# Kernel tuning notes

Hardware: AMD Instinct MI355X
Metric: run time of the kernel (lower is better)

## Reference

```python
import jax, jax.numpy as jnp
import numpy as np

B, T, F, H = 4096, 128, 64, 32
SCALE = 0.05  # small init so relu-LSTM doesn't blow up over 128 steps


def setup_inputs() -> dict:
    key = jax.random.key(0)
    ks = jax.random.split(key, 7)
    return {
        "x": jax.random.normal(ks[0], (B, T, F), jnp.float32),
        "We": jax.random.normal(ks[1], (F, 4 * H), jnp.float32) * SCALE,
        "Ue": jax.random.normal(ks[2], (H, 4 * H), jnp.float32) * SCALE,
        "be": jnp.zeros((4 * H,), jnp.float32),
        "Wd": jax.random.normal(ks[3], (H, 4 * H), jnp.float32) * SCALE,
        "Ud": jax.random.normal(ks[4], (H, 4 * H), jnp.float32) * SCALE,
        "bd": jnp.zeros((4 * H,), jnp.float32),
        "Wout": jax.random.normal(ks[5], (H, F), jnp.float32) * SCALE,
        "bout": jnp.zeros((F,), jnp.float32),
    }


def _lstm_relu(x, W, U, b):
    """Keras LSTM with activation='relu', recurrent_activation='sigmoid'.
    x: [B,T,D]. Returns (h_T [B,H], h_seq [B,T,H]). Gate order: i,f,c,o."""
    Bx = x.shape[0]
    Hh = U.shape[0]
    xz = jnp.einsum('btd,dg->btg', x, W) + b  # precompute input projections

    def step(carry, zt):
        h, c = carry
        z = zt + h @ U
        i, f, g, o = jnp.split(z, 4, axis=-1)
        i = jax.nn.sigmoid(i)
        f = jax.nn.sigmoid(f)
        g = jax.nn.relu(g)
        o = jax.nn.sigmoid(o)
        c = f * c + i * g
        h = o * jax.nn.relu(c)
        return (h, c), h

    h0 = jnp.zeros((Bx, Hh), x.dtype)
    (hT, _), hs = jax.lax.scan(step, (h0, h0), jnp.swapaxes(xz, 0, 1))
    return hT, jnp.swapaxes(hs, 0, 1)


def reference(x, We, Ue, be, Wd, Ud, bd, Wout, bout):
    # Encoder: LSTM(32, relu, return_sequences=False) -> RepeatVector(T)
    hT, _ = _lstm_relu(x, We, Ue, be)                      # [B,H]
    z = jnp.broadcast_to(hT[:, None, :], (x.shape[0], x.shape[1], hT.shape[-1]))
    # Decoder: LSTM(32, relu, return_sequences=True) -> TimeDistributed(Dense(F))
    _, hs = _lstm_relu(z, Wd, Ud, bd)                      # [B,T,H]
    return jnp.einsum('bth,hf->btf', hs, Wout) + bout      # [B,T,F]
```

## Files before the change

### kernel.cpp

```cpp
#include <hip/hip_runtime.h>
#include <hip/hip_bf16.h>

#define B_ 4096
#define T_ 128
#define F_ 64
#define H_ 32
#define G_ 128

using short8 = __attribute__((ext_vector_type(8))) short;
using f32x4  = __attribute__((ext_vector_type(4))) float;
using uint2v = __attribute__((ext_vector_type(2))) unsigned int;
using uint4v = __attribute__((ext_vector_type(4))) unsigned int;

#define MFMA16(Af, Bf, Cf) __builtin_amdgcn_mfma_f32_16x16x32_bf16((Af), (Bf), (Cf), 0, 0, 0)

__device__ __forceinline__ float sigmoid_f(float z) {
    return __builtin_amdgcn_rcpf(1.0f + __expf(-z));
}
__device__ __forceinline__ unsigned short bfb(float f) {
    return __builtin_bit_cast(unsigned short, __float2bfloat16(f));
}
__device__ __forceinline__ unsigned int pk(float a, float b) {
    return (unsigned int)bfb(a) | ((unsigned int)bfb(b) << 16);
}

extern "C" __global__ __launch_bounds__(128, 1)
void lstm_ae(const float* __restrict__ x,
             const float* __restrict__ We,
             const float* __restrict__ Ue,
             const float* __restrict__ be,
             const float* __restrict__ Wd,
             const float* __restrict__ Ud,
             const float* __restrict__ bd,
             const float* __restrict__ Wout,
             const float* __restrict__ bout,
             float* __restrict__ out)
{
    const int lane = threadIdx.x & 63;
    const int rw   = threadIdx.x >> 6;
    const int g    = lane >> 4;
    const int c    = lane & 15;
    const int b0   = blockIdx.x << 4;

    __shared__ __align__(16) unsigned int hx[2][16 * 18];

    short8 weF[4][2];
    short8 ueF[4];
    f32x4  beC[4];
#pragma unroll
    for (int q = 0; q < 4; ++q) {
        const int n = 2 * q + rw;
#pragma unroll
        for (int kc = 0; kc < 2; ++kc)
#pragma unroll
            for (int i = 0; i < 8; ++i)
                weF[q][kc][i] = (short)bfb(We[(kc * 32 + 8 * g + i) * G_ + 16 * n + c]);
#pragma unroll
        for (int i = 0; i < 8; ++i)
            ueF[q][i] = (short)bfb(Ue[(4 * g + (i & 3) + 16 * (i >> 2)) * G_ + 16 * n + c]);
        beC[q] = *(const f32x4*)(be + 16 * n + 4 * g);
    }

    const float* xr = x + (size_t)(b0 + c) * (T_ * F_);
    const int xo = 8 * g;

    short8 hfrag = (short8)0;
    float  cs[4] = {0.f, 0.f, 0.f, 0.f};

#define CVTX(xf0, xf1)                                   \
    {                                                    \
        _Pragma("unroll")                                \
        for (int i = 0; i < 4; ++i) {                    \
            xf0[i]     = (short)bfb(xa[i]);              \
            xf0[4 + i] = (short)bfb(xb[i]);              \
            xf1[i]     = (short)bfb(xc[i]);              \
            xf1[4 + i] = (short)bfb(xd[i]);              \
        }                                                \
    }

#define GATES4(ACC, OWN)                                 \
    {                                                    \
        float hv[4];                                     \
        _Pragma("unroll")                                \
        for (int r = 0; r < 4; ++r) {                    \
            float iv = sigmoid_f(ACC[0][r]);             \
            float fv = sigmoid_f(ACC[1][r]);             \
            float gv = fmaxf(ACC[2][r], 0.f);            \
            float ov = sigmoid_f(ACC[3][r]);             \
            float cc = fmaf(fv, cs[r], iv * gv);         \
            cs[r] = cc;                                  \
            hv[r] = ov * fmaxf(cc, 0.f);                 \
        }                                                \
        OWN.x = pk(hv[0], hv[1]);                        \
        OWN.y = pk(hv[2], hv[3]);                        \
    }

    f32x4 xa = *(const f32x4*)(xr + xo);
    f32x4 xb = *(const f32x4*)(xr + xo + 4);
    f32x4 xc = *(const f32x4*)(xr + 32 + xo);
    f32x4 xd = *(const f32x4*)(xr + 36 + xo);
    short8 xf0, xf1;
    CVTX(xf0, xf1)
    {
        const float* xn = xr + F_;
        xa = *(const f32x4*)(xn + xo);
        xb = *(const f32x4*)(xn + xo + 4);
        xc = *(const f32x4*)(xn + 32 + xo);
        xd = *(const f32x4*)(xn + 36 + xo);
    }
    f32x4 acc[4];
#pragma unroll
    for (int q = 0; q < 4; ++q) {
        acc[q] = MFMA16(weF[q][0], xf0, beC[q]);
        acc[q] = MFMA16(weF[q][1], xf1, acc[q]);
    }

#pragma unroll 1
    for (int t = 0; t < T_; ++t) {
#pragma unroll
        for (int q = 0; q < 4; ++q)
            acc[q] = MFMA16(ueF[q], hfrag, acc[q]);
        uint2v own;
        GATES4(acc, own)
        *(uint2v*)&hx[t & 1][c * 18 + 8 * rw + 2 * g] = own;
        __syncthreads();

        uint2v oth = *(const uint2v*)&hx[t & 1][c * 18 + 8 * (1 - rw) + 2 * g];
        if (t + 1 < T_) {
            CVTX(xf0, xf1)
            if (t + 2 < T_) {
                const float* xn = xr + (t + 2) * F_;
                xa = *(const f32x4*)(xn + xo);
                xb = *(const f32x4*)(xn + xo + 4);
                xc = *(const f32x4*)(xn + 32 + xo);
                xd = *(const f32x4*)(xn + 36 + xo);
            }
#pragma unroll
            for (int q = 0; q < 4; ++q) {
                acc[q] = MFMA16(weF[q][0], xf0, beC[q]);
                acc[q] = MFMA16(weF[q][1], xf1, acc[q]);
            }
        }
        uint4v hb;
        hb.x = rw ? oth.x : own.x;
        hb.y = rw ? oth.y : own.y;
        hb.z = rw ? own.x : oth.x;
        hb.w = rw ? own.y : oth.y;
        hfrag = __builtin_bit_cast(short8, hb);
    }

    short8 udF[4], woF[2];
    f32x4  zd[4], boC[2];
    {
        short8 wdF[4];
#pragma unroll
        for (int q = 0; q < 4; ++q) {
            const int n = 2 * q + rw;
#pragma unroll
            for (int i = 0; i < 8; ++i) {
                const int pr = 4 * g + (i & 3) + 16 * (i >> 2);
                wdF[q][i] = (short)bfb(Wd[pr * G_ + 16 * n + c]);
                udF[q][i] = (short)bfb(Ud[pr * G_ + 16 * n + c]);
            }
        }
#pragma unroll
        for (int q = 0; q < 4; ++q) {
            f32x4 tb = *(const f32x4*)(bd + 16 * (2 * q + rw) + 4 * g);
            zd[q] = MFMA16(wdF[q], hfrag, tb);
        }
#pragma unroll
        for (int mi = 0; mi < 2; ++mi) {
            const int m = 2 * rw + mi;
#pragma unroll
            for (int i = 0; i < 8; ++i)
                woF[mi][i] = (short)bfb(Wout[(4 * g + (i & 3) + 16 * (i >> 2)) * F_ + 16 * m + c]);
            float v = bout[16 * m + c];
            boC[mi][0] = v; boC[mi][1] = v; boC[mi][2] = v; boC[mi][3] = v;
        }
    }

    hfrag = (short8)0;
#pragma unroll
    for (int r = 0; r < 4; ++r) cs[r] = 0.f;

    float* ob[4];
#pragma unroll
    for (int r = 0; r < 4; ++r)
        ob[r] = out + (size_t)(b0 + 4 * g + r) * (T_ * F_) + c;

#pragma unroll 1
    for (int t = 0; t < T_; ++t) {
#pragma unroll
        for (int q = 0; q < 4; ++q)
            acc[q] = MFMA16(udF[q], hfrag, zd[q]);
        uint2v own;
        GATES4(acc, own)
        *(uint2v*)&hx[t & 1][c * 18 + 8 * rw + 2 * g] = own;
        __syncthreads();

        uint2v oth = *(const uint2v*)&hx[t & 1][c * 18 + 8 * (1 - rw) + 2 * g];
        if (t > 0) {
#pragma unroll
            for (int mi = 0; mi < 2; ++mi) {
                f32x4 oac = MFMA16(hfrag, woF[mi], boC[mi]);
                const int m = 2 * rw + mi;
#pragma unroll
                for (int r = 0; r < 4; ++r)
                    ob[r][(t - 1) * F_ + 16 * m] = oac[r];
            }
        }
        uint4v hb;
        hb.x = rw ? oth.x : own.x;
        hb.y = rw ? oth.y : own.y;
        hb.z = rw ? own.x : oth.x;
        hb.w = rw ? own.y : oth.y;
        hfrag = __builtin_bit_cast(short8, hb);
    }
#pragma unroll
    for (int mi = 0; mi < 2; ++mi) {
        f32x4 oac = MFMA16(hfrag, woF[mi], boC[mi]);
        const int m = 2 * rw + mi;
#pragma unroll
        for (int r = 0; r < 4; ++r)
            ob[r][(T_ - 1) * F_ + 16 * m] = oac[r];
    }
}

extern "C" void kernel_launch(void* const* d_in, const int* in_sizes, int n_in,
                              void* d_out, int out_size, void* d_ws, size_t ws_size,
                              hipStream_t stream) {
    (void)in_sizes; (void)n_in; (void)d_ws; (void)ws_size; (void)out_size;
    const float* x    = (const float*)d_in[0];
    const float* We   = (const float*)d_in[1];
    const float* Ue   = (const float*)d_in[2];
    const float* be   = (const float*)d_in[3];
    const float* Wd   = (const float*)d_in[4];
    const float* Ud   = (const float*)d_in[5];
    const float* bd   = (const float*)d_in[6];
    const float* Wout = (const float*)d_in[7];
    const float* bout = (const float*)d_in[8];
    float* out = (float*)d_out;

    dim3 grid(B_ / 16), block(128);
    hipLaunchKernelGGL(lstm_ae, grid, block, 0, stream,
                       x, We, Ue, be, Wd, Ud, bd, Wout, bout, out);
}
```

Before: 392.8 us.

## Split gate nonlinearities across four waves per block with lighter barrier

Raises the block from two to four waves. Each pair of waves computes the same gate MFMAs redundantly, and each wave then evaluates the nonlinearities for only two of the four accumulator rows. This halves the per-wave serial gate and transcendental work on the recurrent critical path. The shared h exchange becomes a single 16-byte read of all four waves' words. The __syncthreads is replaced by an explicit lgkmcnt wait plus s_barrier, and the output projection is split so each wave does one 16-column MFMA. The cost is duplicated MFMA and x-load work, and more registers and waves per block.

```diff
diff --git a/kernel.cpp b/kernel.cpp
--- a/kernel.cpp
+++ b/kernel.cpp
@@ -9,7 +9,6 @@
 
 using short8 = __attribute__((ext_vector_type(8))) short;
 using f32x4  = __attribute__((ext_vector_type(4))) float;
-using uint2v = __attribute__((ext_vector_type(2))) unsigned int;
 using uint4v = __attribute__((ext_vector_type(4))) unsigned int;
 
 #define MFMA16(Af, Bf, Cf) __builtin_amdgcn_mfma_f32_16x16x32_bf16((Af), (Bf), (Cf), 0, 0, 0)
@@ -24,7 +23,14 @@
     return (unsigned int)bfb(a) | ((unsigned int)bfb(b) << 16);
 }
 
-extern "C" __global__ __launch_bounds__(128, 1)
+#define XBAR()                                                  \
+    {                                                           \
+        asm volatile("s_waitcnt lgkmcnt(0)" ::: "memory");      \
+        __builtin_amdgcn_s_barrier();                           \
+        __builtin_amdgcn_sched_barrier(0);                      \
+    }
+
+extern "C" __global__ __launch_bounds__(256, 1)
 void lstm_ae(const float* __restrict__ x,
              const float* __restrict__ We,
              const float* __restrict__ Ue,
@@ -37,19 +43,21 @@
              float* __restrict__ out)
 {
     const int lane = threadIdx.x & 63;
-    const int rw   = threadIdx.x >> 6;
+    const int w    = threadIdx.x >> 6;
+    const int hw   = w >> 1;
+    const int rsel = w & 1;
     const int g    = lane >> 4;
     const int c    = lane & 15;
     const int b0   = blockIdx.x << 4;
 
-    __shared__ __align__(16) unsigned int hx[2][16 * 18];
+    __shared__ __align__(16) unsigned int hx[2][16 * 20];
 
     short8 weF[4][2];
     short8 ueF[4];
     f32x4  beC[4];
 #pragma unroll
     for (int q = 0; q < 4; ++q) {
-        const int n = 2 * q + rw;
+        const int n = 2 * q + hw;
 #pragma unroll
         for (int kc = 0; kc < 2; ++kc)
 #pragma unroll
@@ -65,7 +73,7 @@
     const int xo = 8 * g;
 
     short8 hfrag = (short8)0;
-    float  cs[4] = {0.f, 0.f, 0.f, 0.f};
+    float cs0 = 0.f, cs1 = 0.f;
 
 #define CVTX(xf0, xf1)                                   \
     {                                                    \
@@ -78,22 +86,25 @@
         }                                                \
     }
 
-#define GATES4(ACC, OWN)                                 \
+#define GATES2(R0, R1)                                   \
     {                                                    \
-        float hv[4];                                     \
-        _Pragma("unroll")                                \
-        for (int r = 0; r < 4; ++r) {                    \
-            float iv = sigmoid_f(ACC[0][r]);             \
-            float fv = sigmoid_f(ACC[1][r]);             \
-            float gv = fmaxf(ACC[2][r], 0.f);            \
-            float ov = sigmoid_f(ACC[3][r]);             \
-            float cc = fmaf(fv, cs[r], iv * gv);         \
-            cs[r] = cc;                                  \
-            hv[r] = ov * fmaxf(cc, 0.f);                 \
-        }                                                \
-        OWN.x = pk(hv[0], hv[1]);                        \
-        OWN.y = pk(hv[2], hv[3]);                        \
-    }
+        float iv0 = sigmoid_f(acc[0][R0]);               \
+        float fv0 = sigmoid_f(acc[1][R0]);               \
+        float gv0 = fmaxf(acc[2][R0], 0.f);              \
+        float ov0 = sigmoid_f(acc[3][R0]);               \
+        float cc0 = fmaf(fv0, cs0, iv0 * gv0);           \
+        cs0 = cc0;                                       \
+        float h0 = ov0 * fmaxf(cc0, 0.f);                \
+        float iv1 = sigmoid_f(acc[0][R1]);               \
+        float fv1 = sigmoid_f(acc[1][R1]);               \
+        float gv1 = fmaxf(acc[2][R1], 0.f);              \
+        float ov1 = sigmoid_f(acc[3][R1]);               \
+        float cc1 = fmaf(fv1, cs1, iv1 * gv1);           \
+        cs1 = cc1;                                       \
+        float h1 = ov1 * fmaxf(cc1, 0.f);                \
+        hword = pk(h0, h1);                              \
+    }
+#define GATES()  { if (rsel == 0) GATES2(0, 1) else GATES2(2, 3) }
 
     f32x4 xa = *(const f32x4*)(xr + xo);
     f32x4 xb = *(const f32x4*)(xr + xo + 4);
@@ -120,12 +131,11 @@
 #pragma unroll
         for (int q = 0; q < 4; ++q)
             acc[q] = MFMA16(ueF[q], hfrag, acc[q]);
-        uint2v own;
-        GATES4(acc, own)
-        *(uint2v*)&hx[t & 1][c * 18 + 8 * rw + 2 * g] = own;
-        __syncthreads();
-
-        uint2v oth = *(const uint2v*)&hx[t & 1][c * 18 + 8 * (1 - rw) + 2 * g];
+        unsigned int hword;
+        GATES()
+        hx[t & 1][c * 20 + 4 * g + w] = hword;
+        XBAR()
+        uint4v hb = *(const uint4v*)&hx[t & 1][c * 20 + 4 * g];
         if (t + 1 < T_) {
             CVTX(xf0, xf1)
             if (t + 2 < T_) {
@@ -141,21 +151,16 @@
                 acc[q] = MFMA16(weF[q][1], xf1, acc[q]);
             }
         }
-        uint4v hb;
-        hb.x = rw ? oth.x : own.x;
-        hb.y = rw ? oth.y : own.y;
-        hb.z = rw ? own.x : oth.x;
-        hb.w = rw ? own.y : oth.y;
         hfrag = __builtin_bit_cast(short8, hb);
     }
 
-    short8 udF[4], woF[2];
-    f32x4  zd[4], boC[2];
+    short8 udF[4], woF;
+    f32x4  zd[4], boC;
     {
         short8 wdF[4];
 #pragma unroll
         for (int q = 0; q < 4; ++q) {
-            const int n = 2 * q + rw;
+            const int n = 2 * q + hw;
 #pragma unroll
             for (int i = 0; i < 8; ++i) {
                 const int pr = 4 * g + (i & 3) + 16 * (i >> 2);
@@ -165,64 +170,47 @@
         }
 #pragma unroll
         for (int q = 0; q < 4; ++q) {
-            f32x4 tb = *(const f32x4*)(bd + 16 * (2 * q + rw) + 4 * g);
+            f32x4 tb = *(const f32x4*)(bd + 16 * (2 * q + hw) + 4 * g);
             zd[q] = MFMA16(wdF[q], hfrag, tb);
         }
 #pragma unroll
-        for (int mi = 0; mi < 2; ++mi) {
-            const int m = 2 * rw + mi;
-#pragma unroll
-            for (int i = 0; i < 8; ++i)
-                woF[mi][i] = (short)bfb(Wout[(4 * g + (i & 3) + 16 * (i >> 2)) * F_ + 16 * m + c]);
-            float v = bout[16 * m + c];
-            boC[mi][0] = v; boC[mi][1] = v; boC[mi][2] = v; boC[mi][3] = v;
-        }
+        for (int i = 0; i < 8; ++i)
+            woF[i] = (short)bfb(Wout[(4 * g + (i & 3) + 16 * (i >> 2)) * F_ + 16 * w + c]);
+        float v = bout[16 * w + c];
+        boC[0] = v; boC[1] = v; boC[2] = v; boC[3] = v;
     }
 
     hfrag = (short8)0;
-#pragma unroll
-    for (int r = 0; r < 4; ++r) cs[r] = 0.f;
+    cs0 = 0.f; cs1 = 0.f;
 
     float* ob[4];
 #pragma unroll
     for (int r = 0; r < 4; ++r)
-        ob[r] = out + (size_t)(b0 + 4 * g + r) * (T_ * F_) + c;
+        ob[r] = out + (size_t)(b0 + 4 * g + r) * (T_ * F_) + 16 * w + c;
 
 #pragma unroll 1
     for (int t = 0; t < T_; ++t) {
 #pragma unroll
         for (int q = 0; q < 4; ++q)
             acc[q] = MFMA16(udF[q], hfrag, zd[q]);
-        uint2v own;
-        GATES4(acc, own)
-        *(uint2v*)&hx[t & 1][c * 18 + 8 * rw + 2 * g] = own;
-        __syncthreads();
-
-        uint2v oth = *(const uint2v*)&hx[t & 1][c * 18 + 8 * (1 - rw) + 2 * g];
+        unsigned int hword;
+        GATES()
+        hx[t & 1][c * 20 + 4 * g + w] = hword;
+        XBAR()
+        uint4v hb = *(const uint4v*)&hx[t & 1][c * 20 + 4 * g];
         if (t > 0) {
-#pragma unroll
-            for (int mi = 0; mi < 2; ++mi) {
-                f32x4 oac = MFMA16(hfrag, woF[mi], boC[mi]);
-                const int m = 2 * rw + mi;
-#pragma unroll
-                for (int r = 0; r < 4; ++r)
-                    ob[r][(t - 1) * F_ + 16 * m] = oac[r];
-            }
-        }
-        uint4v hb;
-        hb.x = rw ? oth.x : own.x;
-        hb.y = rw ? oth.y : own.y;
-        hb.z = rw ? own.x : oth.x;
-        hb.w = rw ? own.y : oth.y;
+            f32x4 oac = MFMA16(hfrag, woF, boC);
+#pragma unroll
+            for (int r = 0; r < 4; ++r)
+                ob[r][(t - 1) * F_] = oac[r];
+        }
         hfrag = __builtin_bit_cast(short8, hb);
     }
-#pragma unroll
-    for (int mi = 0; mi < 2; ++mi) {
-        f32x4 oac = MFMA16(hfrag, woF[mi], boC[mi]);
-        const int m = 2 * rw + mi;
+    {
+        f32x4 oac = MFMA16(hfrag, woF, boC);
 #pragma unroll
         for (int r = 0; r < 4; ++r)
-            ob[r][(T_ - 1) * F_ + 16 * m] = oac[r];
+            ob[r][(T_ - 1) * F_] = oac[r];
     }
 }
 
@@ -241,7 +229,7 @@
     const float* bout = (const float*)d_in[8];
     float* out = (float*)d_out;
 
-    dim3 grid(B_ / 16), block(128);
+    dim3 grid(B_ / 16), block(256);
     hipLaunchKernelGGL(lstm_ae, grid, block, 0, stream,
                        x, We, Ue, be, Wd, Ud, bd, Wout, bout, out);
 }
```

After: 408.7 us. 4.1% more time.
